# Kernel optimization log

Measured on AMD Instinct MI355X. Metric: run time of the kernel, lower is better.

Reference implementation:

```python
import jax, jax.numpy as jnp
import numpy as np

# Static sizes (RED-GNN on ICEWS14-like graph)
B = 32          # batch (queries)
N = 100000      # active nodes per layer (fixed frontier size)
E = 1000000     # edges per layer
H = 64          # hidden_dim
A = 5           # attn_dim
L = 3           # n_layer
N_REL = 230
N_ENT = 7128
N_TIME = 365


def setup_inputs() -> dict:
    key = jax.random.key(0)
    ks = jax.random.split(key, 16)
    inp = {}
    # edge structure (constant w.r.t. differentiation)
    inp['batch_idx'] = jax.random.randint(ks[0], (E,), 0, B)
    inp['src_idx'] = jax.random.randint(ks[1], (E,), 0, N)
    inp['dst_idx'] = jax.random.randint(ks[2], (E,), 0, N)
    inp['rel_idx'] = jax.random.randint(ks[3], (E,), 0, N_REL + 1)
    # signed relative time in [-(N_TIME-1), N_TIME-1]
    inp['rel_time'] = jax.random.randint(ks[4], (E,), -(N_TIME - 1), N_TIME)
    inp['query_rel'] = jax.random.randint(ks[5], (B,), 0, N_REL + 1)
    # unique (batch, entity) slot per final node
    n = jnp.arange(N)
    inp['out_batch'] = n // N_ENT
    inp['out_ent'] = n % N_ENT
    # learned parameters
    s = 1.0 / np.sqrt(H)
    inp['rela_embed'] = jax.random.normal(ks[6], (L, N_REL + 1, H), jnp.float32) * s
    inp['time_embed'] = jax.random.normal(ks[7], (N_TIME, H), jnp.float32) * s
    inp['Wp'] = jax.random.normal(ks[8], (H, H), jnp.float32) * s
    inp['Wn'] = jax.random.normal(ks[9], (H, H), jnp.float32) * s
    inp['Wf'] = jax.random.normal(ks[10], (H, H), jnp.float32) * s
    inp['W1'] = jax.random.normal(ks[11], (L, A, 3 * H), jnp.float32) * s
    inp['W2'] = jax.random.normal(ks[12], (L, 1, A), jnp.float32) / np.sqrt(A)
    inp['Wc'] = jax.random.normal(ks[13], (1, H), jnp.float32) * s
    inp['bc'] = jnp.zeros((1,), jnp.float32)
    return inp


def reference(rela_embed, time_embed, Wp, Wn, Wf, W1, W2, Wc, bc,
              batch_idx, src_idx, dst_idx, rel_idx, rel_time,
              query_rel, out_batch, out_ent):
    hidden = jnp.zeros((N, H), dtype=rela_embed.dtype)
    q_rel_e = query_rel[batch_idx]                 # [E]
    t_emb = time_embed[jnp.abs(rel_time)]          # [E,H]
    pos = (rel_time > 0)[:, None]
    zer = (rel_time == 0)[:, None]
    for i in range(L):
        rel_e = rela_embed[i][rel_idx]             # [E,H]
        embed = hidden[src_idx] + rel_e + t_emb    # [E,H]
        # branch by sign of relative time: future / now / past linear
        transformed = jnp.where(pos, embed @ Wf.T,
                      jnp.where(zer, embed @ Wn.T, embed @ Wp.T))
        attn_in = jnp.concatenate(
            [hidden[src_idx], rel_e, rela_embed[i][q_rel_e]], axis=1)  # [E,3H]
        score = jax.nn.sigmoid(
            jax.nn.relu(attn_in @ W1[i].T) @ W2[i].T)  # [E,1]
        msg = score * transformed                      # [E,H]
        hidden = jax.nn.relu(
            jax.ops.segment_sum(msg, dst_idx, num_segments=N))
    result = (hidden @ Wc.T + bc).reshape(-1)          # [N]
    score_all = jnp.zeros((B, N_ENT), result.dtype)
    score_all = score_all.at[out_batch, out_ent].set(result)
    return score_all
```

## Files before the change

### kernel.cpp

```cpp
#include <hip/hip_runtime.h>

#define NB   32
#define NN   100000
#define NE   1000000
#define HD   64
#define AD   5
#define NL   3
#define NRL  231
#define NTM  365
#define NOUT 228096
#define NBLK1 391


__device__ __forceinline__ float bflo(unsigned u) { return __uint_as_float(u << 16); }
__device__ __forceinline__ float bfhi(unsigned u) { return __uint_as_float(u & 0xffff0000u); }
__device__ __forceinline__ unsigned packbf2(float x, float y) {
    unsigned ux = __float_as_uint(x), uy = __float_as_uint(y);
    ux = (ux + 0x7fffu + ((ux >> 16) & 1u)) >> 16;
    uy = (uy + 0x7fffu + ((uy >> 16) & 1u)) >> 16;
    return ux | (uy << 16);
}

__global__ __launch_bounds__(256) void prep_wt_kernel(
    const float* __restrict__ Wp, const float* __restrict__ Wn,
    const float* __restrict__ Wf, float* __restrict__ WT)
{
    int i = blockIdx.x * 256 + threadIdx.x;
    if (i >= 3 * 64 * 64) return;
    int c = i >> 12;
    int k = (i >> 6) & 63;
    int h = i & 63;
    const float* W = (c == 0) ? Wf : (c == 1 ? Wn : Wp);
    WT[i] = W[h * 64 + k];
}

__global__ __launch_bounds__(256) void prep_tables_kernel(
    const float* __restrict__ rela_embed,
    const float* __restrict__ W1,
    float* __restrict__ Trel,
    float* __restrict__ Tq)
{
    int l = blockIdx.x;
    int r = threadIdx.x;
    if (r >= NRL) return;
    const float4* rrow = (const float4*)(rela_embed + ((size_t)l * NRL + r) * HD);
    const float* W1l = W1 + (size_t)l * AD * 192;
    float tr[AD] = {0,0,0,0,0}, tq[AD] = {0,0,0,0,0};
    #pragma unroll
    for (int k4 = 0; k4 < 16; ++k4) {
        float4 x = rrow[k4];
        #pragma unroll
        for (int a = 0; a < AD; ++a) {
            const float* wr = W1l + a * 192 + 64 + k4 * 4;
            const float* wq = W1l + a * 192 + 128 + k4 * 4;
            tr[a] = fmaf(x.x, wr[0], tr[a]); tr[a] = fmaf(x.y, wr[1], tr[a]);
            tr[a] = fmaf(x.z, wr[2], tr[a]); tr[a] = fmaf(x.w, wr[3], tr[a]);
            tq[a] = fmaf(x.x, wq[0], tq[a]); tq[a] = fmaf(x.y, wq[1], tq[a]);
            tq[a] = fmaf(x.z, wq[2], tq[a]); tq[a] = fmaf(x.w, wq[3], tq[a]);
        }
    }
    float* tro = Trel + ((size_t)l * NRL + r) * 8;
    float* tqo = Tq   + ((size_t)l * NRL + r) * 8;
    #pragma unroll
    for (int a = 0; a < AD; ++a) { tro[a] = tr[a]; tqo[a] = tq[a]; }
    tro[5] = tro[6] = tro[7] = 0.f;
    tqo[5] = tqo[6] = tqo[7] = 0.f;
}

__global__ __launch_bounds__(256) void hist_kernel(
    const int* __restrict__ dst_idx, int* __restrict__ deg)
{
    int e = blockIdx.x * 256 + threadIdx.x;
    if (e < NE) atomicAdd(&deg[dst_idx[e]], 1);
}

__global__ __launch_bounds__(256) void scan1_kernel(
    const int* __restrict__ deg, int* __restrict__ tmp, int* __restrict__ bsum)
{
    __shared__ int s[256];
    int tid = threadIdx.x;
    int i = blockIdx.x * 256 + tid;
    int v = (i < NN) ? deg[i] : 0;
    s[tid] = v;
    __syncthreads();
    #pragma unroll
    for (int st = 1; st < 256; st <<= 1) {
        int t = (tid >= st) ? s[tid - st] : 0;
        __syncthreads();
        s[tid] += t;
        __syncthreads();
    }
    if (i < NN) tmp[i] = s[tid];
    if (tid == 255) bsum[blockIdx.x] = s[255];
}

__global__ __launch_bounds__(512) void scan2_kernel(
    const int* __restrict__ bsum, int* __restrict__ bpref)
{
    __shared__ int s[512];
    int tid = threadIdx.x;
    int v = (tid < NBLK1) ? bsum[tid] : 0;
    s[tid] = v;
    __syncthreads();
    #pragma unroll
    for (int st = 1; st < 512; st <<= 1) {
        int t = (tid >= st) ? s[tid - st] : 0;
        __syncthreads();
        s[tid] += t;
        __syncthreads();
    }
    if (tid < NBLK1) bpref[tid] = s[tid] - v;
}

__global__ __launch_bounds__(256) void scan3_kernel(
    const int* __restrict__ deg, const int* __restrict__ tmp,
    const int* __restrict__ bpref, int* __restrict__ off, int* __restrict__ cursor)
{
    int i = blockIdx.x * 256 + threadIdx.x;
    if (i >= NN) return;
    int incl = tmp[i] + bpref[i >> 8];
    off[i + 1] = incl;
    cursor[i] = incl - deg[i];
    if (i == 0) off[0] = 0;
}

__global__ __launch_bounds__(256) void sort_scatter_kernel(
    const int* __restrict__ dst_idx, const int* __restrict__ src_idx,
    const int* __restrict__ rel_idx, const int* __restrict__ rel_time,
    const int* __restrict__ batch_idx, const int* __restrict__ query_rel,
    const float* __restrict__ Trel0, const float* __restrict__ Tq0,
    const float* __restrict__ W2,
    int* __restrict__ cursor, int2* __restrict__ meta,
    float* __restrict__ score0)
{
    int e = blockIdx.x * 256 + threadIdx.x;
    if (e >= NE) return;
    int d = dst_idx[e];
    int rt = rel_time[e];
    int cls = (rt > 0) ? 0 : ((rt == 0) ? 1 : 2);
    int ta = (rt < 0) ? -rt : rt;
    int rel = rel_idx[e];
    int q = query_rel[batch_idx[e]];
    int pos = atomicAdd(&cursor[d], 1);
    int2 m;
    m.x = src_idx[e] | (rel << 17) | (cls << 25);
    m.y = ta | (q << 9);
    meta[pos] = m;

    float4 t0 = *(const float4*)(Trel0 + rel * 8);
    float  t4 = Trel0[rel * 8 + 4];
    float4 u0 = *(const float4*)(Tq0 + q * 8);
    float  u4 = Tq0[q * 8 + 4];
    float z = 0.f;
    z = fmaf(fmaxf(t0.x + u0.x, 0.f), W2[0], z);
    z = fmaf(fmaxf(t0.y + u0.y, 0.f), W2[1], z);
    z = fmaf(fmaxf(t0.z + u0.z, 0.f), W2[2], z);
    z = fmaf(fmaxf(t0.w + u0.w, 0.f), W2[3], z);
    z = fmaf(fmaxf(t4   + u4,   0.f), W2[4], z);
    score0[pos] = 1.f / (1.f + __expf(-z));
}

__global__ __launch_bounds__(256) void score_kernel(
    const float* __restrict__ proj,
    const float* __restrict__ Trel,
    const float* __restrict__ Tq,
    const float* __restrict__ W2,
    const int2* __restrict__ meta,
    float* __restrict__ score)
{
    int j = blockIdx.x * 256 + threadIdx.x;
    if (j >= NE) return;
    int2 mt = meta[j];
    int rel = (mt.x >> 17) & 0xFF;
    int q   = (mt.y >> 9) & 0xFF;
    int src = mt.x & 0x1FFFF;

    float4 t0 = *(const float4*)(Trel + rel * 8);
    float  t4 = Trel[rel * 8 + 4];
    float4 u0 = *(const float4*)(Tq + q * 8);
    float  u4 = Tq[q * 8 + 4];
    float4 p0 = *(const float4*)(proj + (size_t)src * 8);
    float  p4 = proj[(size_t)src * 8 + 4];
    float z = 0.f;
    z = fmaf(fmaxf(p0.x + t0.x + u0.x, 0.f), W2[0], z);
    z = fmaf(fmaxf(p0.y + t0.y + u0.y, 0.f), W2[1], z);
    z = fmaf(fmaxf(p0.z + t0.z + u0.z, 0.f), W2[2], z);
    z = fmaf(fmaxf(p0.w + t0.w + u0.w, 0.f), W2[3], z);
    z = fmaf(fmaxf(p4   + t4   + u4,   0.f), W2[4], z);
    score[j] = 1.f / (1.f + __expf(-z));
}

template <bool HZ>
__device__ __forceinline__ void edge1(
    int2 m, float sc, int hc8,
    const ushort* __restrict__ hidden_in,
    const float* __restrict__ rela, const float* __restrict__ temb,
    float4* __restrict__ A)
{
    int src = m.x & 0x1FFFF, rel = (m.x >> 17) & 0xFF;
    int cl  = (m.x >> 25) & 3, ta = m.y & 511;
    const float* rp = rela + rel * HD + hc8;
    const float* tp = temb + ta * HD + hc8;
    float4 rv0 = *(const float4*)rp;
    float4 rv1 = *(const float4*)(rp + 4);
    float4 tv0 = *(const float4*)tp;
    float4 tv1 = *(const float4*)(tp + 4);
    float4 v0, v1;
    v0.x = rv0.x + tv0.x; v0.y = rv0.y + tv0.y;
    v0.z = rv0.z + tv0.z; v0.w = rv0.w + tv0.w;
    v1.x = rv1.x + tv1.x; v1.y = rv1.y + tv1.y;
    v1.z = rv1.z + tv1.z; v1.w = rv1.w + tv1.w;
    if (!HZ) {
        uint4 hv = *(const uint4*)(hidden_in + (size_t)src * HD + hc8);
        v0.x += bflo(hv.x); v0.y += bfhi(hv.x);
        v0.z += bflo(hv.y); v0.w += bfhi(hv.y);
        v1.x += bflo(hv.z); v1.y += bfhi(hv.z);
        v1.z += bflo(hv.w); v1.w += bfhi(hv.w);
    }
    float sA = (cl == 0) ? sc : 0.f;
    float sB = (cl == 1) ? sc : 0.f;
    float sC = (cl == 2) ? sc : 0.f;
    A[0].x = fmaf(sA, v0.x, A[0].x); A[0].y = fmaf(sA, v0.y, A[0].y);
    A[0].z = fmaf(sA, v0.z, A[0].z); A[0].w = fmaf(sA, v0.w, A[0].w);
    A[1].x = fmaf(sA, v1.x, A[1].x); A[1].y = fmaf(sA, v1.y, A[1].y);
    A[1].z = fmaf(sA, v1.z, A[1].z); A[1].w = fmaf(sA, v1.w, A[1].w);
    A[2].x = fmaf(sB, v0.x, A[2].x); A[2].y = fmaf(sB, v0.y, A[2].y);
    A[2].z = fmaf(sB, v0.z, A[2].z); A[2].w = fmaf(sB, v0.w, A[2].w);
    A[3].x = fmaf(sB, v1.x, A[3].x); A[3].y = fmaf(sB, v1.y, A[3].y);
    A[3].z = fmaf(sB, v1.z, A[3].z); A[3].w = fmaf(sB, v1.w, A[3].w);
    A[4].x = fmaf(sC, v0.x, A[4].x); A[4].y = fmaf(sC, v0.y, A[4].y);
    A[4].z = fmaf(sC, v0.z, A[4].z); A[4].w = fmaf(sC, v0.w, A[4].w);
    A[5].x = fmaf(sC, v1.x, A[5].x); A[5].y = fmaf(sC, v1.y, A[5].y);
    A[5].z = fmaf(sC, v1.z, A[5].z); A[5].w = fmaf(sC, v1.w, A[5].w);
}

#define LPITCH 65
template <bool HZ, bool PROJ>
__global__ __launch_bounds__(256, 4) void reduce_transform_kernel(
    const ushort* __restrict__ hidden_in,
    const float* __restrict__ rela,
    const float* __restrict__ temb,
    const float* __restrict__ score,
    const int2* __restrict__ meta,
    const int*  __restrict__ off,
    const float* __restrict__ WT,
    const float* __restrict__ W1next,
    ushort* __restrict__ hidden_out,
    float* __restrict__ proj_out)
{
    __shared__ float lds_t[64 * LPITCH];
    int tid  = threadIdx.x;
    int lane = tid & 63;
    int w    = __builtin_amdgcn_readfirstlane(tid >> 6);
    int g    = lane >> 3;
    int hc   = lane & 7;
    int hc8  = hc * 8;
    int node0 = blockIdx.x * 64;
    int h0 = w * 16;

    float4 a[2][6];
    #pragma unroll
    for (int rr = 0; rr < 2; ++rr)
        #pragma unroll
        for (int c = 0; c < 6; ++c)
            a[rr][c] = make_float4(0.f, 0.f, 0.f, 0.f);

    #pragma unroll
    for (int rr = 0; rr < 2; ++rr) {
        int nl = w * 16 + rr * 8 + g;
        int node = node0 + nl;
        if (node >= NN) continue;
        int o0 = off[node];
        int o1 = off[node + 1];
        int j = o0;
        for (; j + 2 <= o1; j += 2) {
            int2 m0 = meta[j], m1 = meta[j + 1];
            float s0 = score[j], s1 = score[j + 1];
            edge1<HZ>(m0, s0, hc8, hidden_in, rela, temb, a[rr]);
            edge1<HZ>(m1, s1, hc8, hidden_in, rela, temb, a[rr]);
        }
        if (j < o1)
            edge1<HZ>(meta[j], score[j], hc8, hidden_in, rela, temb, a[rr]);
    }

    float acc[16];
    #pragma unroll
    for (int i = 0; i < 16; ++i) acc[i] = 0.f;

    #pragma unroll
    for (int c = 0; c < 3; ++c) {
        __syncthreads();
        #pragma unroll
        for (int rr = 0; rr < 2; ++rr) {
            int nl = w * 16 + rr * 8 + g;
            float4 lo = a[rr][2 * c];
            float4 hi = a[rr][2 * c + 1];
            lds_t[(hc8 + 0) * LPITCH + nl] = lo.x;
            lds_t[(hc8 + 1) * LPITCH + nl] = lo.y;
            lds_t[(hc8 + 2) * LPITCH + nl] = lo.z;
            lds_t[(hc8 + 3) * LPITCH + nl] = lo.w;
            lds_t[(hc8 + 4) * LPITCH + nl] = hi.x;
            lds_t[(hc8 + 5) * LPITCH + nl] = hi.y;
            lds_t[(hc8 + 6) * LPITCH + nl] = hi.z;
            lds_t[(hc8 + 7) * LPITCH + nl] = hi.w;
        }
        __syncthreads();
        const float* __restrict__ Wb = WT + (c * 64) * 64 + h0;
        #pragma unroll 4
        for (int k = 0; k < 64; ++k) {
            float av = lds_t[k * LPITCH + lane];
            #pragma unroll
            for (int i = 0; i < 16; ++i)
                acc[i] = fmaf(av, Wb[k * 64 + i], acc[i]);
        }
    }

    int node = node0 + lane;
    if (node < NN) {
        ushort* outp = hidden_out + (size_t)node * 64 + h0;
        unsigned up[8];
        #pragma unroll
        for (int p = 0; p < 8; ++p)
            up[p] = packbf2(fmaxf(acc[2 * p], 0.f), fmaxf(acc[2 * p + 1], 0.f));
        *(uint4*)(outp)     = make_uint4(up[0], up[1], up[2], up[3]);
        *(uint4*)(outp + 8) = make_uint4(up[4], up[5], up[6], up[7]);
    }

    if (PROJ) {
        float pa[AD];
        #pragma unroll
        for (int aa = 0; aa < AD; ++aa) pa[aa] = 0.f;
        #pragma unroll
        for (int i = 0; i < 16; ++i) {
            float hv = fmaxf(acc[i], 0.f);
            #pragma unroll
            for (int aa = 0; aa < AD; ++aa)
                pa[aa] = fmaf(hv, W1next[aa * 192 + h0 + i], pa[aa]);
        }
        __syncthreads();
        float* lds2 = lds_t;
        #pragma unroll
        for (int aa = 0; aa < AD; ++aa)
            lds2[(w * 64 + lane) * AD + aa] = pa[aa];
        __syncthreads();
        for (int idx = tid; idx < 64 * 8; idx += 256) {
            int nd = idx >> 3, aa = idx & 7;
            if (node0 + nd >= NN) break;
            float v = 0.f;
            if (aa < AD) {
                #pragma unroll
                for (int w4 = 0; w4 < 4; ++w4)
                    v += lds2[(w4 * 64 + nd) * AD + aa];
            }
            proj_out[(size_t)(node0 + nd) * 8 + aa] = v;
        }
    }
}

__global__ __launch_bounds__(256) void out_kernel(
    const ushort* __restrict__ hidden,
    const float* __restrict__ Wc,
    const float* __restrict__ bc,
    float* __restrict__ out)
{
    int i = blockIdx.x * 256 + threadIdx.x;
    if (i >= NOUT) return;
    float r = 0.f;
    if (i < NN) {
        const uint4* h4 = (const uint4*)(hidden + (size_t)i * 64);
        float acc = 0.f;
        #pragma unroll
        for (int q = 0; q < 8; ++q) {
            uint4 hv = h4[q];
            const float* wq = Wc + q * 8;
            acc = fmaf(bflo(hv.x), wq[0], acc);
            acc = fmaf(bfhi(hv.x), wq[1], acc);
            acc = fmaf(bflo(hv.y), wq[2], acc);
            acc = fmaf(bfhi(hv.y), wq[3], acc);
            acc = fmaf(bflo(hv.z), wq[4], acc);
            acc = fmaf(bfhi(hv.z), wq[5], acc);
            acc = fmaf(bflo(hv.w), wq[6], acc);
            acc = fmaf(bfhi(hv.w), wq[7], acc);
        }
        r = acc + bc[0];
    }
    out[i] = r;
}

extern "C" void kernel_launch(void* const* d_in, const int* in_sizes, int n_in,
                              void* d_out, int out_size, void* d_ws, size_t ws_size,
                              hipStream_t stream)
{
    const int*   batch_idx  = (const int*)d_in[0];
    const int*   src_idx    = (const int*)d_in[1];
    const int*   dst_idx    = (const int*)d_in[2];
    const int*   rel_idx    = (const int*)d_in[3];
    const int*   rel_time   = (const int*)d_in[4];
    const int*   query_rel  = (const int*)d_in[5];
    const float* rela_embed = (const float*)d_in[8];
    const float* time_embed = (const float*)d_in[9];
    const float* Wp         = (const float*)d_in[10];
    const float* Wn         = (const float*)d_in[11];
    const float* Wf         = (const float*)d_in[12];
    const float* W1         = (const float*)d_in[13];
    const float* W2         = (const float*)d_in[14];
    const float* Wc         = (const float*)d_in[15];
    const float* bc         = (const float*)d_in[16];
    float* out = (float*)d_out;

    char* ws = (char*)d_ws;
    ushort* hid0  = (ushort*)(ws + 0);
    ushort* hid1  = (ushort*)(ws + 12800000);
    float* projA  = (float*)(ws + 25600000);
    float* projB  = (float*)(ws + 28800000);
    float* score  = (float*)(ws + 32000000);
    float* WT     = (float*)(ws + 36000000);
    float* Trel   = (float*)(ws + 36100000);
    float* Tq     = (float*)(ws + 36130000);
    int*   off    = (int*)  (ws + 36160000);
    int2*  meta   = (int2*) (ws + 37400000);
    int*   deg    = (int*)  (ws + 45400000);
    int*   tmp    = (int*)  (ws + 46600000);
    int*   cursor = (int*)  (ws + 47800000);
    int*   bsum   = (int*)  (ws + 49000000);
    int*   bpref  = (int*)  (ws + 49010000);

    prep_wt_kernel<<<48, 256, 0, stream>>>(Wp, Wn, Wf, WT);
    prep_tables_kernel<<<NL, 256, 0, stream>>>(rela_embed, W1, Trel, Tq);

    hipMemsetAsync(deg, 0, NN * sizeof(int), stream);
    hist_kernel<<<(NE + 255) / 256, 256, 0, stream>>>(dst_idx, deg);
    scan1_kernel<<<NBLK1, 256, 0, stream>>>(deg, tmp, bsum);
    scan2_kernel<<<1, 512, 0, stream>>>(bsum, bpref);
    scan3_kernel<<<NBLK1, 256, 0, stream>>>(deg, tmp, bpref, off, cursor);
    sort_scatter_kernel<<<(NE + 255) / 256, 256, 0, stream>>>(
        dst_idx, src_idx, rel_idx, rel_time, batch_idx, query_rel,
        Trel, Tq, W2, cursor, meta, score);

    int grid = (NN + 63) / 64;
    int sgrid = (NE + 255) / 256;
    {
        reduce_transform_kernel<true, true><<<grid, 256, 0, stream>>>(
            hid1, rela_embed, time_embed, score, meta, off,
            WT, W1 + (size_t)1 * AD * 192, hid0, projA);
    }
    {
        const float* rela = rela_embed + (size_t)1 * NRL * HD;
        score_kernel<<<sgrid, 256, 0, stream>>>(
            projA, Trel + (size_t)1 * NRL * 8, Tq + (size_t)1 * NRL * 8,
            W2 + 1 * AD, meta, score);
        reduce_transform_kernel<false, true><<<grid, 256, 0, stream>>>(
            hid0, rela, time_embed, score, meta, off,
            WT, W1 + (size_t)2 * AD * 192, hid1, projB);
    }
    {
        const float* rela = rela_embed + (size_t)2 * NRL * HD;
        score_kernel<<<sgrid, 256, 0, stream>>>(
            projB, Trel + (size_t)2 * NRL * 8, Tq + (size_t)2 * NRL * 8,
            W2 + 2 * AD, meta, score);
        reduce_transform_kernel<false, false><<<grid, 256, 0, stream>>>(
            hid1, rela, time_embed, score, meta, off,
            WT, nullptr, hid0, nullptr);
    }

    out_kernel<<<(NOUT + 255) / 256, 256, 0, stream>>>(hid0, Wc, bc, out);
}
```

Baseline: 466.7 us.

## Sort nodes by in-degree to balance edge loops across wave lanes

Builds a degree histogram, scans it, and scatters node ids into a permutation ordered by descending in-degree. The reduce-transform kernels then process nodes in that order, so each wave groups nodes with similar edge counts. The aim is to cut intra-wave divergence from uneven per-node edge loops. In exchange it adds three small preprocessing kernels with contended atomics, plus indirect, scattered hidden and projection writes.

Result: slower. 1.080 ms (+131.5%).

```diff
diff --git a/kernel.cpp b/kernel.cpp
--- a/kernel.cpp
+++ b/kernel.cpp
@@ -10,6 +10,7 @@
 #define NTM  365
 #define NOUT 228096
 #define NBLK1 391
+#define NDBIN 1024
 
 
 __device__ __forceinline__ float bflo(unsigned u) { return __uint_as_float(u << 16); }
@@ -114,14 +115,47 @@
 
 __global__ __launch_bounds__(256) void scan3_kernel(
     const int* __restrict__ deg, const int* __restrict__ tmp,
-    const int* __restrict__ bpref, int* __restrict__ off, int* __restrict__ cursor)
+    const int* __restrict__ bpref, int* __restrict__ off, int* __restrict__ cursor,
+    int* __restrict__ dhist)
 {
     int i = blockIdx.x * 256 + threadIdx.x;
     if (i >= NN) return;
+    int d = deg[i];
     int incl = tmp[i] + bpref[i >> 8];
     off[i + 1] = incl;
-    cursor[i] = incl - deg[i];
+    cursor[i] = incl - d;
     if (i == 0) off[0] = 0;
+    int bin = (d < NDBIN) ? d : (NDBIN - 1);
+    atomicAdd(&dhist[bin], 1);
+}
+
+__global__ __launch_bounds__(1024) void dscan_kernel(
+    const int* __restrict__ dhist, int* __restrict__ dcur)
+{
+    __shared__ int s[NDBIN];
+    int tid = threadIdx.x;
+    int v = dhist[tid];
+    s[tid] = v;
+    __syncthreads();
+    #pragma unroll
+    for (int st = 1; st < NDBIN; st <<= 1) {
+        int t = (tid >= st) ? s[tid - st] : 0;
+        __syncthreads();
+        s[tid] += t;
+        __syncthreads();
+    }
+    dcur[tid] = NN - s[tid];
+}
+
+__global__ __launch_bounds__(256) void dscatter_kernel(
+    const int* __restrict__ deg, int* __restrict__ dcur, int* __restrict__ perm)
+{
+    int n = blockIdx.x * 256 + threadIdx.x;
+    if (n >= NN) return;
+    int d = deg[n];
+    int bin = (d < NDBIN) ? d : (NDBIN - 1);
+    int pos = atomicAdd(&dcur[bin], 1);
+    perm[pos] = n;
 }
 
 __global__ __launch_bounds__(256) void sort_scatter_kernel(
@@ -243,6 +277,7 @@
     const float* __restrict__ score,
     const int2* __restrict__ meta,
     const int*  __restrict__ off,
+    const int*  __restrict__ perm,
     const float* __restrict__ WT,
     const float* __restrict__ W1next,
     ushort* __restrict__ hidden_out,
@@ -267,9 +302,9 @@
 
     #pragma unroll
     for (int rr = 0; rr < 2; ++rr) {
-        int nl = w * 16 + rr * 8 + g;
-        int node = node0 + nl;
-        if (node >= NN) continue;
+        int pidx = node0 + w * 16 + rr * 8 + g;
+        if (pidx >= NN) continue;
+        int node = perm[pidx];
         int o0 = off[node];
         int o1 = off[node + 1];
         int j = o0;
@@ -315,8 +350,9 @@
         }
     }
 
-    int node = node0 + lane;
-    if (node < NN) {
+    int pl = node0 + lane;
+    if (pl < NN) {
+        int node = perm[pl];
         ushort* outp = hidden_out + (size_t)node * 64 + h0;
         unsigned up[8];
         #pragma unroll
@@ -352,7 +388,7 @@
                 for (int w4 = 0; w4 < 4; ++w4)
                     v += lds2[(w4 * 64 + nd) * AD + aa];
             }
-            proj_out[(size_t)(node0 + nd) * 8 + aa] = v;
+            proj_out[(size_t)perm[node0 + nd] * 8 + aa] = v;
         }
     }
 }
@@ -424,15 +460,21 @@
     int*   cursor = (int*)  (ws + 47800000);
     int*   bsum   = (int*)  (ws + 49000000);
     int*   bpref  = (int*)  (ws + 49010000);
+    int*   dhist  = (int*)  (ws + 49020000);
+    int*   dcur   = (int*)  (ws + 49030000);
+    int*   perm   = (int*)  (ws + 49040000);
 
     prep_wt_kernel<<<48, 256, 0, stream>>>(Wp, Wn, Wf, WT);
     prep_tables_kernel<<<NL, 256, 0, stream>>>(rela_embed, W1, Trel, Tq);
 
     hipMemsetAsync(deg, 0, NN * sizeof(int), stream);
+    hipMemsetAsync(dhist, 0, NDBIN * sizeof(int), stream);
     hist_kernel<<<(NE + 255) / 256, 256, 0, stream>>>(dst_idx, deg);
     scan1_kernel<<<NBLK1, 256, 0, stream>>>(deg, tmp, bsum);
     scan2_kernel<<<1, 512, 0, stream>>>(bsum, bpref);
-    scan3_kernel<<<NBLK1, 256, 0, stream>>>(deg, tmp, bpref, off, cursor);
+    scan3_kernel<<<NBLK1, 256, 0, stream>>>(deg, tmp, bpref, off, cursor, dhist);
+    dscan_kernel<<<1, NDBIN, 0, stream>>>(dhist, dcur);
+    dscatter_kernel<<<NBLK1, 256, 0, stream>>>(deg, dcur, perm);
     sort_scatter_kernel<<<(NE + 255) / 256, 256, 0, stream>>>(
         dst_idx, src_idx, rel_idx, rel_time, batch_idx, query_rel,
         Trel, Tq, W2, cursor, meta, score);
@@ -441,7 +483,7 @@
     int sgrid = (NE + 255) / 256;
     {
         reduce_transform_kernel<true, true><<<grid, 256, 0, stream>>>(
-            hid1, rela_embed, time_embed, score, meta, off,
+            hid1, rela_embed, time_embed, score, meta, off, perm,
             WT, W1 + (size_t)1 * AD * 192, hid0, projA);
     }
     {
@@ -450,7 +492,7 @@
             projA, Trel + (size_t)1 * NRL * 8, Tq + (size_t)1 * NRL * 8,
             W2 + 1 * AD, meta, score);
         reduce_transform_kernel<false, true><<<grid, 256, 0, stream>>>(
-            hid0, rela, time_embed, score, meta, off,
+            hid0, rela, time_embed, score, meta, off, perm,
             WT, W1 + (size_t)2 * AD * 192, hid1, projB);
     }
     {
@@ -459,7 +501,7 @@
             projB, Trel + (size_t)2 * NRL * 8, Tq + (size_t)2 * NRL * 8,
             W2 + 2 * AD, meta, score);
         reduce_transform_kernel<false, false><<<grid, 256, 0, stream>>>(
-            hid1, rela, time_embed, score, meta, off,
+            hid1, rela, time_embed, score, meta, off, perm,
             WT, nullptr, hid0, nullptr);
     }
 
```
